# Kernel tuning notes

Hardware: AMD Instinct MI355X
Metric: run time of the kernel (lower is better)

## Reference

```python
import jax, jax.numpy as jnp
import numpy as np

B, T, C = 4, 2048, 1024
H, D = 16, 64           # num_heads, head_size
R = D // 2              # rotary_ndims = 32


def _make_rope(T, R):
    # RotaryEmbedding(dim=R): inv_freq over arange(0, R, 2)
    inv_freq = 1.0 / (10000.0 ** (np.arange(0, R, 2, dtype=np.float32) / R))
    t = np.arange(T, dtype=np.float32)
    freqs = np.einsum('i,j->ij', t, inv_freq)        # [T, R/2]
    emb = np.concatenate([freqs, freqs], axis=-1)    # [T, R]
    return jnp.asarray(np.stack([np.cos(emb), np.sin(emb)]), dtype=jnp.float32)  # [2, T, R]


def setup_inputs() -> dict:
    key = jax.random.key(0)
    ks = jax.random.split(key, 10)
    s = 1.0 / np.sqrt(C)
    inp = {
        'x': jax.random.normal(ks[0], (B, T, C), dtype=jnp.float32),
        'RoPE': _make_rope(T, R),
        'key_padding_mask': jax.random.randint(ks[1], (B, T), 0, 2, dtype=jnp.int32),
        'Wq': jax.random.normal(ks[2], (C, C), dtype=jnp.float32) * s,
        'bq': jnp.zeros((C,), dtype=jnp.float32),
        'Wk': jax.random.normal(ks[3], (C, C), dtype=jnp.float32) * s,
        'bk': jnp.zeros((C,), dtype=jnp.float32),
        'Wv': jax.random.normal(ks[4], (C, C), dtype=jnp.float32) * s,
        'bv': jnp.zeros((C,), dtype=jnp.float32),
        'Wo': jax.random.normal(ks[5], (C, C), dtype=jnp.float32) * s,
        'bo': jnp.zeros((C,), dtype=jnp.float32),
    }
    return inp


def _rotate_half(x):
    x1, x2 = x[..., : x.shape[-1] // 2], x[..., x.shape[-1] // 2:]
    return jnp.concatenate([-x2, x1], axis=-1)


def reference(x, RoPE, key_padding_mask, Wq, bq, Wk, bk, Wv, bv, Wo, bo):
    Bx, Tx, Cx = x.shape
    # projections -> [B, H, T, D]
    def proj(W, b):
        return (x @ W.T + b).reshape(Bx, Tx, H, D).transpose(0, 2, 1, 3)
    q, k, v = proj(Wq, bq), proj(Wk, bk), proj(Wv, bv)

    # partial rotary: first R dims rotated, rest passed through
    q_rot, q_pass = q[..., :R], q[..., R:]
    k_rot, k_pass = k[..., :R], k[..., R:]
    cos, sin = RoPE[0][:Tx], RoPE[1][:Tx]            # [T, R]
    q_rot = q_rot * cos + _rotate_half(q_rot) * sin
    k_rot = k_rot * cos + _rotate_half(k_rot) * sin
    q = jnp.concatenate([q_rot, q_pass], axis=-1)
    k = jnp.concatenate([k_rot, k_pass], axis=-1)

    att = jnp.einsum('bhqd,bhkd->bhqk', q, k) * (1.0 / np.sqrt(D))
    mask = key_padding_mask[:, None, None, :]        # [B,1,1,T]
    att = jnp.where(mask == 0, jnp.asarray(-1e30, att.dtype), att)
    att = jax.nn.softmax(att, axis=-1)
    out = jnp.einsum('bhqk,bhkd->bhqd', att, v)      # [B,H,T,D]
    out = out.transpose(0, 2, 1, 3).reshape(Bx, Tx, Cx)
    return out @ Wo.T + bo
```

## Files before the change

### kernel.cpp

```cpp
#include <hip/hip_runtime.h>
#include <stdint.h>


typedef __attribute__((ext_vector_type(8))) short bf16x8;
typedef __attribute__((ext_vector_type(4))) float f32x4;
typedef __attribute__((ext_vector_type(4))) short short4v;
typedef __attribute__((ext_vector_type(2))) uint32_t uint2v;

#define MFMA16(a, b, c) __builtin_amdgcn_mfma_f32_16x16x32_bf16((a), (b), (c), 0, 0, 0)

#if __has_builtin(__builtin_amdgcn_exp2f)
#define FEXP(x) __builtin_amdgcn_exp2f(x)
#define QSCALE 0.18033688011112042f
#else
#define FEXP(x) __expf(x)
#define QSCALE 0.125f
#endif

static __device__ __forceinline__ short f2bf(float f) {
  union { float fv; uint32_t u; } v; v.fv = f;
  uint32_t r = v.u + 0x7FFFu + ((v.u >> 16) & 1u);
  return (short)(r >> 16);
}

static __device__ __forceinline__ uint32_t pack_trunc(float a, float b) {
  union { float f; uint32_t u; } ua, ub;
  ua.f = a; ub.f = b;
#if __has_builtin(__builtin_amdgcn_perm)
  return __builtin_amdgcn_perm(ub.u, ua.u, 0x07060302u);
#else
  return (ub.u & 0xFFFF0000u) | (ua.u >> 16);
#endif
}

typedef __attribute__((address_space(1))) void as1_void;
typedef __attribute__((address_space(3))) void as3_void;
static __device__ __forceinline__ void gld_lds16(const void* g, void* l) {
  __builtin_amdgcn_global_load_lds((as1_void*)g, (as3_void*)l, 16, 0, 0);
}

__global__ __launch_bounds__(256) void cvt_kernel(
    const float* x, const float* wq, const float* wk, const float* wv,
    const float* wo,
    short* xb, short* wqb, short* wkb, short* wvb, short* wob) {
  int64_t g = (int64_t)blockIdx.x * 256 + threadIdx.x;
  const int64_t NX = 8388608 / 4, NW = 1048576 / 4;
  const float* src;
  short* dst;
  int64_t i;
  if (g < NX)               { src = x;  dst = xb;  i = g; }
  else if (g < NX + NW)     { src = wq; dst = wqb; i = g - NX; }
  else if (g < NX + 2 * NW) { src = wk; dst = wkb; i = g - NX - NW; }
  else if (g < NX + 3 * NW) { src = wv; dst = wvb; i = g - NX - 2 * NW; }
  else                      { src = wo; dst = wob; i = g - NX - 3 * NW; }
  float4 v = ((const float4*)src)[i];
  short4v o;
  o[0] = f2bf(v.x); o[1] = f2bf(v.y); o[2] = f2bf(v.z); o[3] = f2bf(v.w);
  *(short4v*)&dst[i * 4] = o;
}

__global__ __launch_bounds__(256) void qkv_gemm(
    const short* __restrict__ Xb,
    const short* __restrict__ Wq, const short* __restrict__ Wk,
    const short* __restrict__ Wv,
    const float* __restrict__ bq, const float* __restrict__ bk,
    const float* __restrict__ bv,
    const float* __restrict__ rope, const int* __restrict__ mask,
    short* __restrict__ Qh, short* __restrict__ Kh, short* __restrict__ Vt) {
  __shared__ __align__(16) short As[128 * 32];
  __shared__ __align__(16) short Bs[128 * 32];

  const int t = threadIdx.x;
  const int lane = t & 63;
  const int wave = t >> 6;
  const int c = lane & 15;
  const int quad = lane >> 4;
  const int m0 = blockIdx.x * 128;
  const int n0 = blockIdx.y * 128;
  const int mat = blockIdx.z;
  const short* Wg = (mat == 0) ? Wq : (mat == 1) ? Wk : Wv;
  const float* bias = (mat == 0) ? bq : (mat == 1) ? bk : bv;

  f32x4 zero4 = {0.f, 0.f, 0.f, 0.f};
  f32x4 acc[4][4];
#pragma unroll
  for (int i = 0; i < 4; ++i)
#pragma unroll
    for (int j = 0; j < 4; ++j) acc[i][j] = zero4;

  const int wm = wave & 1, wn = wave >> 1;

  const int srow = t >> 2;
  const int gc = ((t & 3) - (srow >> 2)) & 3;
  const short* gA = Xb + (size_t)(m0 + srow) * 1024 + gc * 8;
  const short* gB = Wg + (size_t)(n0 + srow) * 1024 + gc * 8;
  short* lA = &As[t * 8];
  short* lB = &Bs[t * 8];

  for (int k0 = 0; k0 < 1024; k0 += 32) {
    gld_lds16(gA + k0, lA);
    gld_lds16(gA + k0 + 65536, lA + 2048);
    gld_lds16(gB + k0, lB);
    gld_lds16(gB + k0 + 65536, lB + 2048);
    __syncthreads();

    bf16x8 af[4], bfr[4];
#pragma unroll
    for (int i = 0; i < 4; ++i) {
      int mr = wm * 64 + i * 16 + c;
      af[i] = *(const bf16x8*)&As[mr * 32 + (((quad + (mr >> 2)) & 3) * 8)];
      int nr = wn * 64 + i * 16 + c;
      bfr[i] = *(const bf16x8*)&Bs[nr * 32 + (((quad + (nr >> 2)) & 3) * 8)];
    }
#pragma unroll
    for (int i = 0; i < 4; ++i)
#pragma unroll
      for (int j = 0; j < 4; ++j) acc[i][j] = MFMA16(af[i], bfr[j], acc[i][j]);
    __syncthreads();
  }

  const int nb = n0 + wn * 64;
  const int hcol = nb >> 6;
  float bj[4];
#pragma unroll
  for (int j = 0; j < 4; ++j) bj[j] = bias[nb + j * 16 + c];
  const int bidx = m0 >> 11;
  const int tbase = (m0 & 2047) + wm * 64 + quad * 4;
  const int* mrow = mask + bidx * 2048;

  if (mat < 2) {
    short* Og = (mat == 0) ? Qh : Kh;
    size_t hb = (size_t)(bidx * 16 + hcol) * 2048;
#pragma unroll
    for (int i = 0; i < 4; ++i) {
#pragma unroll
      for (int r = 0; r < 4; ++r) {
        int tp = tbase + i * 16 + r;
        float f = (mat == 0) ? QSCALE : (mrow[tp] ? 1.0f : 0.0f);
        float cosv = rope[tp * 32 + c];
        float sinv = rope[65536 + tp * 32 + c];
        float v0 = acc[i][0][r] + bj[0];
        float v1 = acc[i][1][r] + bj[1];
        float v2 = acc[i][2][r] + bj[2];
        float v3 = acc[i][3][r] + bj[3];
        size_t base = (hb + tp) * 64;
        Og[base + c]      = f2bf((v0 * cosv - v1 * sinv) * f);
        Og[base + 16 + c] = f2bf((v1 * cosv + v0 * sinv) * f);
        Og[base + 32 + c] = f2bf(v2 * f);
        Og[base + 48 + c] = f2bf(v3 * f);
      }
    }
  } else {
    size_t hb = (size_t)(bidx * 16 + hcol) * 64;
#pragma unroll
    for (int i = 0; i < 4; ++i) {
      int tp = tbase + i * 16;
      int4 mv = *(const int4*)&mrow[tp];
      float fr[4];
      fr[0] = mv.x ? 1.f : 0.f; fr[1] = mv.y ? 1.f : 0.f;
      fr[2] = mv.z ? 1.f : 0.f; fr[3] = mv.w ? 1.f : 0.f;
#pragma unroll
      for (int j = 0; j < 4; ++j) {
        short4v pv;
#pragma unroll
        for (int r = 0; r < 4; ++r) pv[r] = f2bf((acc[i][j][r] + bj[j]) * fr[r]);
        size_t base = (hb + j * 16 + c) * 2048 + tp;
        *(short4v*)&Vt[base] = pv;
      }
    }
  }
}

__global__ __launch_bounds__(256, 4) void attn_kernel(
    const short* __restrict__ Qh, const short* __restrict__ Kh,
    const short* __restrict__ Vt, const int* __restrict__ mask,
    short* __restrict__ Og) {
  __shared__ __align__(16) short Ks[64 * 64];
  __shared__ __align__(16) short Vs[64 * 64];
  __shared__ __align__(16) short Pl[4][32 * 64];
  __shared__ float nmw[4];

  const int t = threadIdx.x;
  const int lane = t & 63;
  const int wave = t >> 6;
  const int c = lane & 15;
  const int quad = lane >> 4;
  const int qt = blockIdx.x;
  const int bh = blockIdx.y;
  const int bidx = bh >> 4;
  const short* Qg = Qh + ((size_t)bh * 2048 + qt * 128) * 64;
  const short* Kg = Kh + (size_t)bh * 2048 * 64;
  const short* Vg = Vt + (size_t)bh * 64 * 2048;

  {
    const int4* mr = (const int4*)(mask + bidx * 2048);
    int4 a = mr[t * 2], b = mr[t * 2 + 1];
    int cnt = (a.x == 0) + (a.y == 0) + (a.z == 0) + (a.w == 0) +
              (b.x == 0) + (b.y == 0) + (b.z == 0) + (b.w == 0);
    cnt += __shfl_xor(cnt, 1);  cnt += __shfl_xor(cnt, 2);
    cnt += __shfl_xor(cnt, 4);  cnt += __shfl_xor(cnt, 8);
    cnt += __shfl_xor(cnt, 16); cnt += __shfl_xor(cnt, 32);
    if (lane == 0) nmw[wave] = (float)cnt;
  }

  bf16x8 qf[2][2];
#pragma unroll
  for (int ks = 0; ks < 2; ++ks)
#pragma unroll
    for (int it = 0; it < 2; ++it)
      qf[ks][it] =
          *(const bf16x8*)&Qg[(wave * 32 + it * 16 + c) * 64 + ks * 32 + quad * 8];

  const bf16x8 ones = {0x3F80, 0x3F80, 0x3F80, 0x3F80,
                       0x3F80, 0x3F80, 0x3F80, 0x3F80};

  f32x4 zero4 = {0.f, 0.f, 0.f, 0.f};
  f32x4 O[4][2];
#pragma unroll
  for (int dt = 0; dt < 4; ++dt)
#pragma unroll
    for (int it = 0; it < 2; ++it) O[dt][it] = zero4;
  f32x4 Ol[2] = {zero4, zero4};

  const int krow0 = t >> 3;
  const int klc = (t & 7) ^ (krow0 & 7);
  const short* gk0 = Kg + (size_t)krow0 * 64 + klc * 8;
  const short* gv0 = Vg + (size_t)krow0 * 2048 + klc * 8;
  short* Pw = &Pl[wave][0];

  for (int c0 = 0; c0 < 2048; c0 += 64) {
    gld_lds16(gk0 + (size_t)c0 * 64, &Ks[t * 8]);
    gld_lds16(gk0 + (size_t)(c0 + 32) * 64, &Ks[t * 8 + 2048]);
    gld_lds16(gv0 + c0, &Vs[t * 8]);
    gld_lds16(gv0 + c0 + 32 * 2048, &Vs[t * 8 + 2048]);
    __syncthreads();

    f32x4 St[4][2];
#pragma unroll
    for (int jt = 0; jt < 4; ++jt) {
      bf16x8 ak =
          *(const bf16x8*)&Ks[(jt * 16 + c) * 64 + ((quad ^ (c & 7)) * 8)];
      St[jt][0] = MFMA16(ak, qf[0][0], zero4);
      St[jt][1] = MFMA16(ak, qf[0][1], zero4);
    }
#pragma unroll
    for (int jt = 0; jt < 4; ++jt) {
      bf16x8 ak =
          *(const bf16x8*)&Ks[(jt * 16 + c) * 64 + (((4 + quad) ^ (c & 7)) * 8)];
      St[jt][0] = MFMA16(ak, qf[1][0], St[jt][0]);
      St[jt][1] = MFMA16(ak, qf[1][1], St[jt][1]);
    }

#pragma unroll
    for (int it = 0; it < 2; ++it) {
#pragma unroll
      for (int jt = 0; jt < 4; ++jt) {
        float p0 = FEXP(St[jt][it][0]);
        float p1 = FEXP(St[jt][it][1]);
        float p2 = FEXP(St[jt][it][2]);
        float p3 = FEXP(St[jt][it][3]);
        uint2v pk;
        pk[0] = pack_trunc(p0, p1);
        pk[1] = pack_trunc(p2, p3);
        *(uint2v*)&Pw[(it * 16 + c) * 64 +
                      (((jt * 2 + (quad >> 1)) ^ (c & 7)) * 8) + (quad & 1) * 4] = pk;
      }
    }
    asm volatile("s_waitcnt lgkmcnt(0)" ::: "memory");

#pragma unroll
    for (int ks = 0; ks < 2; ++ks) {
      bf16x8 bp0 = *(const bf16x8*)&Pw[c * 64 + (((ks * 4 + quad) ^ (c & 7)) * 8)];
      bf16x8 bp1 =
          *(const bf16x8*)&Pw[(16 + c) * 64 + (((ks * 4 + quad) ^ (c & 7)) * 8)];
      Ol[0] = MFMA16(ones, bp0, Ol[0]);
      Ol[1] = MFMA16(ones, bp1, Ol[1]);
#pragma unroll
      for (int dt = 0; dt < 4; ++dt) {
        bf16x8 av =
            *(const bf16x8*)&Vs[(dt * 16 + c) * 64 + (((4 * ks + quad) ^ (c & 7)) * 8)];
        O[dt][0] = MFMA16(av, bp0, O[dt][0]);
        O[dt][1] = MFMA16(av, bp1, O[dt][1]);
      }
    }
    __syncthreads();
  }

  float nm = nmw[0] + nmw[1] + nmw[2] + nmw[3];
#pragma unroll
  for (int it = 0; it < 2; ++it) {
    float inv = 1.0f / (Ol[it][0] - nm);
    int tq = qt * 128 + wave * 32 + it * 16 + c;
    size_t rb = ((size_t)bidx * 2048 + tq) * 1024 + (size_t)(bh & 15) * 64;
#pragma unroll
    for (int dt = 0; dt < 4; ++dt) {
      short4v ov;
#pragma unroll
      for (int r = 0; r < 4; ++r) ov[r] = f2bf(O[dt][it][r] * inv);
      *(short4v*)&Og[rb + dt * 16 + quad * 4] = ov;
    }
  }
}

__global__ __launch_bounds__(256) void out_gemm(
    const short* __restrict__ Ab, const short* __restrict__ Wob,
    const float* __restrict__ bo, float* __restrict__ out) {
  __shared__ __align__(16) short As[64 * 32];
  __shared__ __align__(16) short Bs[128 * 32];

  const int t = threadIdx.x;
  const int lane = t & 63;
  const int wave = t >> 6;
  const int c = lane & 15;
  const int quad = lane >> 4;
  const int m0 = blockIdx.x * 64;
  const int n0 = blockIdx.y * 128;

  f32x4 zero4 = {0.f, 0.f, 0.f, 0.f};
  f32x4 acc[4][2];
#pragma unroll
  for (int i = 0; i < 4; ++i) {
    acc[i][0] = zero4;
    acc[i][1] = zero4;
  }

  const int srow = t >> 2;
  const int gc = ((t & 3) - (srow >> 2)) & 3;
  const short* gA = Ab + (size_t)(m0 + srow) * 1024 + gc * 8;
  const short* gB = Wob + (size_t)(n0 + srow) * 1024 + gc * 8;

  for (int k0 = 0; k0 < 1024; k0 += 32) {
    gld_lds16(gA + k0, &As[t * 8]);
    gld_lds16(gB + k0, &Bs[t * 8]);
    gld_lds16(gB + k0 + 65536, &Bs[t * 8 + 2048]);
    __syncthreads();

    bf16x8 af[4], bfr[2];
#pragma unroll
    for (int i = 0; i < 4; ++i) {
      int mr = i * 16 + c;
      af[i] = *(const bf16x8*)&As[mr * 32 + (((quad + (mr >> 2)) & 3) * 8)];
    }
#pragma unroll
    for (int j = 0; j < 2; ++j) {
      int nr = wave * 32 + j * 16 + c;
      bfr[j] = *(const bf16x8*)&Bs[nr * 32 + (((quad + (nr >> 2)) & 3) * 8)];
    }
#pragma unroll
    for (int i = 0; i < 4; ++i) {
      acc[i][0] = MFMA16(af[i], bfr[0], acc[i][0]);
      acc[i][1] = MFMA16(af[i], bfr[1], acc[i][1]);
    }
    __syncthreads();
  }

  const int nb = n0 + wave * 32;
  float bj[2];
  bj[0] = bo[nb + c];
  bj[1] = bo[nb + 16 + c];
#pragma unroll
  for (int i = 0; i < 4; ++i) {
    int m = m0 + i * 16 + quad * 4;
#pragma unroll
    for (int r = 0; r < 4; ++r) {
      float* orow = out + (size_t)(m + r) * 1024 + nb;
      orow[c]      = acc[i][0][r] + bj[0];
      orow[16 + c] = acc[i][1][r] + bj[1];
    }
  }
}

extern "C" void kernel_launch(void* const* d_in, const int* in_sizes, int n_in,
                              void* d_out, int out_size, void* d_ws,
                              size_t ws_size, hipStream_t stream) {
  const float* x    = (const float*)d_in[0];
  const float* rope = (const float*)d_in[1];
  const int*   mask = (const int*)d_in[2];
  const float* Wq   = (const float*)d_in[3];
  const float* bq   = (const float*)d_in[4];
  const float* Wk   = (const float*)d_in[5];
  const float* bk   = (const float*)d_in[6];
  const float* Wv   = (const float*)d_in[7];
  const float* bv   = (const float*)d_in[8];
  const float* Wo   = (const float*)d_in[9];
  const float* bo   = (const float*)d_in[10];
  float* out = (float*)d_out;

  char* ws = (char*)d_ws;
  short* xb  = (short*)(ws);
  short* wqb = (short*)(ws + 16777216);
  short* wkb = (short*)(ws + 18874368);
  short* wvb = (short*)(ws + 20971520);
  short* wob = (short*)(ws + 23068672);
  short* Qh  = (short*)(ws + 25198592);
  short* Kh  = (short*)(ws + 41975808);
  short* Vt  = (short*)(ws + 58753024);
  short* att = xb;

  cvt_kernel<<<12288, 256, 0, stream>>>(x, Wq, Wk, Wv, Wo, xb, wqb, wkb, wvb,
                                        wob);
  qkv_gemm<<<dim3(64, 8, 3), 256, 0, stream>>>(xb, wqb, wkb, wvb, bq, bk, bv,
                                               rope, mask, Qh, Kh, Vt);
  attn_kernel<<<dim3(16, 64), 256, 0, stream>>>(Qh, Kh, Vt, mask, att);
  out_gemm<<<dim3(128, 8), 256, 0, stream>>>(att, wob, bo, out);
}
```

Baseline: 295.0 us.

## Double-buffer K/V tiles and double query rows per attention block

```diff
diff --git a/kernel.cpp b/kernel.cpp
--- a/kernel.cpp
+++ b/kernel.cpp
@@ -171,12 +171,12 @@
   }
 }
 
-__global__ __launch_bounds__(256, 4) void attn_kernel(
+__global__ __launch_bounds__(256, 2) void attn_kernel(
     const short* __restrict__ Qh, const short* __restrict__ Kh,
     const short* __restrict__ Vt, const int* __restrict__ mask,
     short* __restrict__ Og) {
-  __shared__ __align__(16) short Ks[64 * 64];
-  __shared__ __align__(16) short Vs[64 * 64];
+  __shared__ __align__(16) short Ks[2][64 * 64];
+  __shared__ __align__(16) short Vs[2][64 * 64];
   __shared__ __align__(16) short Pl[4][32 * 64];
   __shared__ float nmw[4];
 
@@ -188,7 +188,7 @@
   const int qt = blockIdx.x;
   const int bh = blockIdx.y;
   const int bidx = bh >> 4;
-  const short* Qg = Qh + ((size_t)bh * 2048 + qt * 128) * 64;
+  const short* Qg = Qh + ((size_t)bh * 2048 + qt * 256) * 64;
   const short* Kg = Kh + (size_t)bh * 2048 * 64;
   const short* Vg = Vt + (size_t)bh * 64 * 2048;
 
@@ -203,24 +203,24 @@
     if (lane == 0) nmw[wave] = (float)cnt;
   }
 
-  bf16x8 qf[2][2];
+  bf16x8 qf[2][4];
 #pragma unroll
   for (int ks = 0; ks < 2; ++ks)
 #pragma unroll
-    for (int it = 0; it < 2; ++it)
+    for (int it = 0; it < 4; ++it)
       qf[ks][it] =
-          *(const bf16x8*)&Qg[(wave * 32 + it * 16 + c) * 64 + ks * 32 + quad * 8];
+          *(const bf16x8*)&Qg[(wave * 64 + it * 16 + c) * 64 + ks * 32 + quad * 8];
 
   const bf16x8 ones = {0x3F80, 0x3F80, 0x3F80, 0x3F80,
                        0x3F80, 0x3F80, 0x3F80, 0x3F80};
 
   f32x4 zero4 = {0.f, 0.f, 0.f, 0.f};
-  f32x4 O[4][2];
+  f32x4 O[4][4];
 #pragma unroll
   for (int dt = 0; dt < 4; ++dt)
 #pragma unroll
-    for (int it = 0; it < 2; ++it) O[dt][it] = zero4;
-  f32x4 Ol[2] = {zero4, zero4};
+    for (int it = 0; it < 4; ++it) O[dt][it] = zero4;
+  f32x4 Ol[4] = {zero4, zero4, zero4, zero4};
 
   const int krow0 = t >> 3;
   const int klc = (t & 7) ^ (krow0 & 7);
@@ -228,69 +228,84 @@
   const short* gv0 = Vg + (size_t)krow0 * 2048 + klc * 8;
   short* Pw = &Pl[wave][0];
 
-  for (int c0 = 0; c0 < 2048; c0 += 64) {
-    gld_lds16(gk0 + (size_t)c0 * 64, &Ks[t * 8]);
-    gld_lds16(gk0 + (size_t)(c0 + 32) * 64, &Ks[t * 8 + 2048]);
-    gld_lds16(gv0 + c0, &Vs[t * 8]);
-    gld_lds16(gv0 + c0 + 32 * 2048, &Vs[t * 8 + 2048]);
+  gld_lds16(gk0, &Ks[0][t * 8]);
+  gld_lds16(gk0 + 32 * 64, &Ks[0][t * 8 + 2048]);
+  gld_lds16(gv0, &Vs[0][t * 8]);
+  gld_lds16(gv0 + 32 * 2048, &Vs[0][t * 8 + 2048]);
+
+  for (int ci = 0; ci < 32; ++ci) {
     __syncthreads();
-
-    f32x4 St[4][2];
-#pragma unroll
-    for (int jt = 0; jt < 4; ++jt) {
-      bf16x8 ak =
-          *(const bf16x8*)&Ks[(jt * 16 + c) * 64 + ((quad ^ (c & 7)) * 8)];
-      St[jt][0] = MFMA16(ak, qf[0][0], zero4);
-      St[jt][1] = MFMA16(ak, qf[0][1], zero4);
-    }
-#pragma unroll
-    for (int jt = 0; jt < 4; ++jt) {
-      bf16x8 ak =
-          *(const bf16x8*)&Ks[(jt * 16 + c) * 64 + (((4 + quad) ^ (c & 7)) * 8)];
-      St[jt][0] = MFMA16(ak, qf[1][0], St[jt][0]);
-      St[jt][1] = MFMA16(ak, qf[1][1], St[jt][1]);
-    }
-
-#pragma unroll
-    for (int it = 0; it < 2; ++it) {
+    if (ci < 31) {
+      int cn = (ci + 1) * 64;
+      int nb = (ci + 1) & 1;
+      gld_lds16(gk0 + (size_t)cn * 64, &Ks[nb][t * 8]);
+      gld_lds16(gk0 + (size_t)(cn + 32) * 64, &Ks[nb][t * 8 + 2048]);
+      gld_lds16(gv0 + cn, &Vs[nb][t * 8]);
+      gld_lds16(gv0 + cn + 32 * 2048, &Vs[nb][t * 8 + 2048]);
+    }
+    const short* ksb = &Ks[ci & 1][0];
+    const short* vsb = &Vs[ci & 1][0];
+
+#pragma unroll
+    for (int h = 0; h < 2; ++h) {
+      f32x4 St[4][2];
 #pragma unroll
       for (int jt = 0; jt < 4; ++jt) {
-        float p0 = FEXP(St[jt][it][0]);
-        float p1 = FEXP(St[jt][it][1]);
-        float p2 = FEXP(St[jt][it][2]);
-        float p3 = FEXP(St[jt][it][3]);
-        uint2v pk;
-        pk[0] = pack_trunc(p0, p1);
-        pk[1] = pack_trunc(p2, p3);
-        *(uint2v*)&Pw[(it * 16 + c) * 64 +
-                      (((jt * 2 + (quad >> 1)) ^ (c & 7)) * 8) + (quad & 1) * 4] = pk;
-      }
-    }
-    asm volatile("s_waitcnt lgkmcnt(0)" ::: "memory");
-
-#pragma unroll
-    for (int ks = 0; ks < 2; ++ks) {
-      bf16x8 bp0 = *(const bf16x8*)&Pw[c * 64 + (((ks * 4 + quad) ^ (c & 7)) * 8)];
-      bf16x8 bp1 =
-          *(const bf16x8*)&Pw[(16 + c) * 64 + (((ks * 4 + quad) ^ (c & 7)) * 8)];
-      Ol[0] = MFMA16(ones, bp0, Ol[0]);
-      Ol[1] = MFMA16(ones, bp1, Ol[1]);
-#pragma unroll
-      for (int dt = 0; dt < 4; ++dt) {
-        bf16x8 av =
-            *(const bf16x8*)&Vs[(dt * 16 + c) * 64 + (((4 * ks + quad) ^ (c & 7)) * 8)];
-        O[dt][0] = MFMA16(av, bp0, O[dt][0]);
-        O[dt][1] = MFMA16(av, bp1, O[dt][1]);
-      }
-    }
-    __syncthreads();
+        bf16x8 ak =
+            *(const bf16x8*)&ksb[(jt * 16 + c) * 64 + ((quad ^ (c & 7)) * 8)];
+        St[jt][0] = MFMA16(ak, qf[0][h * 2 + 0], zero4);
+        St[jt][1] = MFMA16(ak, qf[0][h * 2 + 1], zero4);
+      }
+#pragma unroll
+      for (int jt = 0; jt < 4; ++jt) {
+        bf16x8 ak =
+            *(const bf16x8*)&ksb[(jt * 16 + c) * 64 + (((4 + quad) ^ (c & 7)) * 8)];
+        St[jt][0] = MFMA16(ak, qf[1][h * 2 + 0], St[jt][0]);
+        St[jt][1] = MFMA16(ak, qf[1][h * 2 + 1], St[jt][1]);
+      }
+
+#pragma unroll
+      for (int itl = 0; itl < 2; ++itl) {
+#pragma unroll
+        for (int jt = 0; jt < 4; ++jt) {
+          float p0 = FEXP(St[jt][itl][0]);
+          float p1 = FEXP(St[jt][itl][1]);
+          float p2 = FEXP(St[jt][itl][2]);
+          float p3 = FEXP(St[jt][itl][3]);
+          uint2v pk;
+          pk[0] = pack_trunc(p0, p1);
+          pk[1] = pack_trunc(p2, p3);
+          *(uint2v*)&Pw[(itl * 16 + c) * 64 +
+                        (((jt * 2 + (quad >> 1)) ^ (c & 7)) * 8) +
+                        (quad & 1) * 4] = pk;
+        }
+      }
+      asm volatile("s_waitcnt lgkmcnt(0)" ::: "memory");
+
+#pragma unroll
+      for (int ks = 0; ks < 2; ++ks) {
+        bf16x8 bp0 =
+            *(const bf16x8*)&Pw[c * 64 + (((ks * 4 + quad) ^ (c & 7)) * 8)];
+        bf16x8 bp1 =
+            *(const bf16x8*)&Pw[(16 + c) * 64 + (((ks * 4 + quad) ^ (c & 7)) * 8)];
+        Ol[h * 2 + 0] = MFMA16(ones, bp0, Ol[h * 2 + 0]);
+        Ol[h * 2 + 1] = MFMA16(ones, bp1, Ol[h * 2 + 1]);
+#pragma unroll
+        for (int dt = 0; dt < 4; ++dt) {
+          bf16x8 av =
+              *(const bf16x8*)&vsb[(dt * 16 + c) * 64 + (((4 * ks + quad) ^ (c & 7)) * 8)];
+          O[dt][h * 2 + 0] = MFMA16(av, bp0, O[dt][h * 2 + 0]);
+          O[dt][h * 2 + 1] = MFMA16(av, bp1, O[dt][h * 2 + 1]);
+        }
+      }
+    }
   }
 
   float nm = nmw[0] + nmw[1] + nmw[2] + nmw[3];
 #pragma unroll
-  for (int it = 0; it < 2; ++it) {
+  for (int it = 0; it < 4; ++it) {
     float inv = 1.0f / (Ol[it][0] - nm);
-    int tq = qt * 128 + wave * 32 + it * 16 + c;
+    int tq = qt * 256 + wave * 64 + it * 16 + c;
     size_t rb = ((size_t)bidx * 2048 + tq) * 1024 + (size_t)(bh & 15) * 64;
 #pragma unroll
     for (int dt = 0; dt < 4; ++dt) {
@@ -401,6 +416,6 @@
                                         wob);
   qkv_gemm<<<dim3(64, 8, 3), 256, 0, stream>>>(xb, wqb, wkb, wvb, bq, bk, bv,
                                                rope, mask, Qh, Kh, Vt);
-  attn_kernel<<<dim3(16, 64), 256, 0, stream>>>(Qh, Kh, Vt, mask, att);
+  attn_kernel<<<dim3(8, 64), 256, 0, stream>>>(Qh, Kh, Vt, mask, att);
   out_gemm<<<dim3(128, 8), 256, 0, stream>>>(att, wob, bo, out);
 }
```

After: 298.9 us. No clear change (+1.3%).
